# Kernel optimization log

Measured on AMD Instinct MI355X. Metric: run time of the kernel, lower is better.

The kernel has to match this reference:

```python
import jax, jax.numpy as jnp
import numpy as np

N, IN_DIM, HID, OUT_DIM, H = 4096, 256, 256, 256, 2
E_RAND = 131072
BN_EPS = 1e-5


def _bn(h, gamma, beta):
    # BatchNorm1d training-mode math: batch mean, biased variance
    mu = jnp.mean(h, axis=0)
    var = jnp.var(h, axis=0)
    return (h - mu) * jax.lax.rsqrt(var + BN_EPS) * gamma + beta


def setup_inputs() -> dict:
    key = jax.random.key(0)
    ks = jax.random.split(key, 16)
    x = jax.random.normal(ks[0], (N, IN_DIM), jnp.float32)
    # random edges + self loops (self loops guarantee every row has >=1 neighbor)
    rnd = jax.random.randint(ks[1], (2, E_RAND), 0, N, jnp.int64)
    loops = jnp.stack([jnp.arange(N, dtype=jnp.int64)] * 2)
    edge_index = jnp.concatenate([rnd, loops], axis=1)
    s = 1.0 / np.sqrt(IN_DIM)
    sh = 1.0 / np.sqrt(HID)
    return {
        "x": x,
        "edge_index": edge_index,
        "wq": jax.random.uniform(ks[2], (IN_DIM, HID), jnp.float32, -s, s),
        "bq": jnp.zeros((HID,), jnp.float32),
        "wk": jax.random.uniform(ks[3], (IN_DIM, HID), jnp.float32, -s, s),
        "bk": jnp.zeros((HID,), jnp.float32),
        "wv": jax.random.uniform(ks[4], (IN_DIM, HID), jnp.float32, -s, s),
        "bv": jnp.zeros((HID,), jnp.float32),
        "wo": jax.random.uniform(ks[5], (HID, IN_DIM), jnp.float32, -sh, sh),
        "bo": jnp.zeros((IN_DIM,), jnp.float32),
        "eps": jnp.zeros((1, 1), jnp.float32),
        "w1": jax.random.uniform(ks[6], (IN_DIM, HID), jnp.float32, -s, s),
        "b1": jnp.zeros((HID,), jnp.float32),
        "g1": jnp.ones((HID,), jnp.float32),
        "be1": jnp.zeros((HID,), jnp.float32),
        "w2": jax.random.uniform(ks[7], (HID, OUT_DIM), jnp.float32, -sh, sh),
        "b2": jnp.zeros((OUT_DIM,), jnp.float32),
        "g2": jnp.ones((OUT_DIM,), jnp.float32),
        "be2": jnp.zeros((OUT_DIM,), jnp.float32),
    }


def reference(x, edge_index, wq, bq, wk, bk, wv, bv, wo, bo, eps,
              w1, b1, g1, be1, w2, b2, g2, be2):
    n = x.shape[0]
    hd = HID // H
    q = (x @ wq + bq).reshape(n, H, hd)
    k = (x @ wk + bk).reshape(n, H, hd)
    v = (x @ wv + bv).reshape(n, H, hd)
    scores = jnp.einsum('nhd,mhd->nhm', q, k) / (hd ** 0.5)  # [n,H,n]
    row, col = edge_index[0], edge_index[1]
    mask = jnp.zeros((n, H, n), bool).at[row, :, col].set(True)
    scores = jnp.where(mask, scores, -jnp.inf)
    attn = jax.nn.softmax(scores, axis=-1)
    v_agg = jnp.einsum('nhm,mhd->nhd', attn, v).reshape(n, HID)
    v_agg = v_agg @ wo + bo + eps * x
    h = jax.nn.relu(_bn(v_agg @ w1 + b1, g1, be1))
    h = jax.nn.relu(_bn(h @ w2 + b2, g2, be2))
    return h  # dropout is identity (eval)
```

## Files before the change

### kernel.cpp

```cpp
#include <hip/hip_runtime.h>
#include <math.h>

#define N_NODES 4096
#define DIM 256
#define GK 256
#define MWORDS 128
#define MAXNBR 192

typedef float f32x4 __attribute__((ext_vector_type(4)));
typedef short s16x8 __attribute__((ext_vector_type(8)));
typedef short s16x4 __attribute__((ext_vector_type(4)));

__device__ __forceinline__ unsigned short bf16_rne(float f) {
  unsigned int u = __float_as_uint(f);
  u += 0x7FFFu + ((u >> 16) & 1u);
  return (unsigned short)(u >> 16);
}

__device__ __forceinline__ void split_bf16(float f, short& hi, short& lo) {
  unsigned short h = bf16_rne(f);
  float hf = __uint_as_float(((unsigned int)h) << 16);
  hi = (short)h;
  lo = (short)bf16_rne(f - hf);
}

__device__ __forceinline__ int swz(int row, int col) {
  return row * 64 + (col ^ ((row & 7) << 3));
}

__global__ void prep_kernel(const int* __restrict__ ei, int E, int nmb,
                            unsigned int* __restrict__ mask,
                            const float* __restrict__ wq, const float* __restrict__ wk,
                            const float* __restrict__ wv, const float* __restrict__ wo,
                            const float* __restrict__ w1, const float* __restrict__ w2,
                            const float* __restrict__ bq, const float* __restrict__ bk,
                            const float* __restrict__ bv,
                            short* __restrict__ wt_hi, short* __restrict__ wt_lo,
                            float* __restrict__ bqkv, float* __restrict__ stats) {
  const int b = blockIdx.x;
  const int t = threadIdx.x;
  if (b < nmb) {
    const int e = b * 256 + t;
    if (e < E) {
      const int r = ei[e];
      const int c = ei[E + e];
      atomicOr(&mask[(size_t)r * MWORDS + (c >> 5)], 1u << (c & 31));
    }
    return;
  }
  const int b2 = b - nmb;
  if (b2 < 1536) {
    const int mat = b2 >> 8;
    const int n = b2 & 255;
    const float* src = (mat == 0) ? wq : (mat == 1) ? wk : (mat == 2) ? wv
                     : (mat == 3) ? wo : (mat == 4) ? w1 : w2;
    const float v = src[(size_t)t * 256 + n];
    short hi, lo;
    split_bf16(v, hi, lo);
    const int nbase = (mat < 3) ? mat * 256 : 768 + (mat - 3) * 256;
    const size_t idx = (size_t)(nbase + n) * GK + t;
    wt_hi[idx] = hi;
    wt_lo[idx] = lo;
    if (t == 0 && mat < 3)
      bqkv[mat * 256 + n] = (mat == 0 ? bq : mat == 1 ? bk : bv)[n];
    return;
  }
  stats[t] = 0.f;
  stats[t + 256] = 0.f;
  stats[t + 512] = 0.f;
  stats[t + 768] = 0.f;
}

template <int EPI, bool BN_IN, bool STATS_OUT>
__launch_bounds__(256)
__global__ void gemm_mfma(const float* __restrict__ A,
                          const short* __restrict__ Wt_hi,
                          const short* __restrict__ Wt_lo,
                          const float* __restrict__ bias,
                          float* __restrict__ C, int ldc,
                          const float* __restrict__ X,
                          const float* __restrict__ epsp,
                          const float* __restrict__ bnsum,
                          const float* __restrict__ bnsq,
                          const float* __restrict__ bng,
                          const float* __restrict__ bnbe,
                          float* __restrict__ osum,
                          float* __restrict__ osq) {
  __shared__ short As_hi[64 * 64], As_lo[64 * 64];
  __shared__ short Bs_hi[64 * 64], Bs_lo[64 * 64];
  __shared__ __align__(16) float bnsc[256], bnsh[256];
  __shared__ float redS[2][2][16], redQ[2][2][16];

  const int tid = threadIdx.x;
  const int lane = tid & 63;
  const int wave = tid >> 6;
  const int wr = wave >> 1, wc = wave & 1;
  const int m0 = blockIdx.y * 64;
  const int n0 = blockIdx.x * 64;
  const int l15 = lane & 15;
  const int lg = lane >> 4;

  if (BN_IN) {
    const float invn = 1.f / (float)N_NODES;
    const float mu = bnsum[tid] * invn;
    const float var = bnsq[tid] * invn - mu * mu;
    const float s = bng[tid] * rsqrtf(var + 1e-5f);
    bnsc[tid] = s;
    bnsh[tid] = fmaf(-mu, s, bnbe[tid]);
  }

  f32x4 acc[2][2] = {};

  for (int kt = 0; kt < GK; kt += 64) {
    __syncthreads();
#pragma unroll
    for (int i = 0; i < 4; ++i) {
      const int row = (tid >> 4) + i * 16;
      const int kc = (tid & 15) * 4;
      float4 av = *(const float4*)(A + (size_t)(m0 + row) * GK + kt + kc);
      if (EPI == 2) {
        const float4 s4 = *(const float4*)&bnsc[kt + kc];
        const float4 h4 = *(const float4*)&bnsh[kt + kc];
        av.x = fmaxf(fmaf(av.x, s4.x, h4.x), 0.f);
        av.y = fmaxf(fmaf(av.y, s4.y, h4.y), 0.f);
        av.z = fmaxf(fmaf(av.z, s4.z, h4.z), 0.f);
        av.w = fmaxf(fmaf(av.w, s4.w, h4.w), 0.f);
      }
      short h0, l0, h1, l1, h2, l2, h3, l3;
      split_bf16(av.x, h0, l0);
      split_bf16(av.y, h1, l1);
      split_bf16(av.z, h2, l2);
      split_bf16(av.w, h3, l3);
      s16x4 hv = {h0, h1, h2, h3};
      s16x4 lv = {l0, l1, l2, l3};
      const int o = swz(row, kc);
      *(s16x4*)&As_hi[o] = hv;
      *(s16x4*)&As_lo[o] = lv;
    }
#pragma unroll
    for (int i = 0; i < 2; ++i) {
      const int row = (tid >> 3) + i * 32;
      const int kc = (tid & 7) * 8;
      s16x8 bh = *(const s16x8*)(Wt_hi + (size_t)(n0 + row) * GK + kt + kc);
      s16x8 bl = *(const s16x8*)(Wt_lo + (size_t)(n0 + row) * GK + kt + kc);
      const int o = swz(row, kc);
      *(s16x8*)&Bs_hi[o] = bh;
      *(s16x8*)&Bs_lo[o] = bl;
    }
    __syncthreads();
#pragma unroll
    for (int kk = 0; kk < 2; ++kk) {
      s16x8 ah[2], al[2], bh[2], bl[2];
#pragma unroll
      for (int f = 0; f < 2; ++f) {
        const int ao = swz(wr * 32 + f * 16 + l15, kk * 32 + lg * 8);
        const int bo = swz(wc * 32 + f * 16 + l15, kk * 32 + lg * 8);
        ah[f] = *(const s16x8*)&As_hi[ao];
        al[f] = *(const s16x8*)&As_lo[ao];
        bh[f] = *(const s16x8*)&Bs_hi[bo];
        bl[f] = *(const s16x8*)&Bs_lo[bo];
      }
#pragma unroll
      for (int fm = 0; fm < 2; ++fm)
#pragma unroll
        for (int fn = 0; fn < 2; ++fn) {
          acc[fm][fn] = __builtin_amdgcn_mfma_f32_16x16x32_bf16(ah[fm], bh[fn], acc[fm][fn], 0, 0, 0);
          acc[fm][fn] = __builtin_amdgcn_mfma_f32_16x16x32_bf16(ah[fm], bl[fn], acc[fm][fn], 0, 0, 0);
          acc[fm][fn] = __builtin_amdgcn_mfma_f32_16x16x32_bf16(al[fm], bh[fn], acc[fm][fn], 0, 0, 0);
        }
    }
  }

  const float ev = (EPI == 1) ? epsp[0] : 0.f;
  float ps[2] = {0.f, 0.f}, pq[2] = {0.f, 0.f};
#pragma unroll
  for (int fm = 0; fm < 2; ++fm) {
    const int row0 = m0 + wr * 32 + fm * 16 + lg * 4;
#pragma unroll
    for (int fn = 0; fn < 2; ++fn) {
      const int col = n0 + wc * 32 + fn * 16 + l15;
      const float bb = bias[col];
#pragma unroll
      for (int j = 0; j < 4; ++j) {
        float v = acc[fm][fn][j] + bb;
        if (EPI == 1) v = fmaf(ev, X[(size_t)(row0 + j) * DIM + col], v);
        C[(size_t)(row0 + j) * ldc + col] = v;
        if (STATS_OUT) {
          ps[fn] += v;
          pq[fn] = fmaf(v, v, pq[fn]);
        }
      }
    }
  }
  if (STATS_OUT) {
#pragma unroll
    for (int fn = 0; fn < 2; ++fn) {
      ps[fn] += __shfl_xor(ps[fn], 16);
      ps[fn] += __shfl_xor(ps[fn], 32);
      pq[fn] += __shfl_xor(pq[fn], 16);
      pq[fn] += __shfl_xor(pq[fn], 32);
    }
    if (wr == 1 && lane < 16) {
      redS[wc][0][l15] = ps[0];
      redS[wc][1][l15] = ps[1];
      redQ[wc][0][l15] = pq[0];
      redQ[wc][1][l15] = pq[1];
    }
    __syncthreads();
    if (wr == 0 && lane < 16) {
#pragma unroll
      for (int fn = 0; fn < 2; ++fn) {
        const int col = n0 + wc * 32 + fn * 16 + l15;
        atomicAdd(&osum[col], ps[fn] + redS[wc][fn][l15]);
        atomicAdd(&osq[col], pq[fn] + redQ[wc][fn][l15]);
      }
    }
  }
}

__launch_bounds__(256)
__global__ void attn_kernel(const float* __restrict__ qkv,
                            const unsigned int* __restrict__ mask,
                            float* __restrict__ vagg) {
  __shared__ int nbr[4][MAXNBR];
  const int wave = threadIdx.x >> 6;
  const int lane = threadIdx.x & 63;
  const int r = blockIdx.x * 4 + wave;

  const unsigned int* mrow = mask + (size_t)r * MWORDS;
  int total = 0;
#pragma unroll
  for (int round = 0; round < 2; ++round) {
    unsigned int w = mrow[round * 64 + lane];
    const int cnt = __popc(w);
    int pre = cnt;
#pragma unroll
    for (int off = 1; off < 64; off <<= 1) {
      int tt = __shfl_up(pre, off);
      if (lane >= off) pre += tt;
    }
    const int wtot = __shfl(pre, 63);
    pre -= cnt;
    int base = total + pre;
    while (w) {
      const int b = __ffs(w) - 1;
      w &= w - 1;
      nbr[wave][base++] = (round * 64 + lane) * 32 + b;
    }
    total += wtot;
  }

  float4 q = *(const float4*)(qkv + (size_t)r * 768 + lane * 4);
  const float sc = 0.088388347648318447f;
  q.x *= sc; q.y *= sc; q.z *= sc; q.w *= sc;

  float4 acc = make_float4(0.f, 0.f, 0.f, 0.f);
  float m = -INFINITY, lsum = 0.f;
  const int* nb = nbr[wave];

  for (int i = 0; i < total; i += 8) {
    int cs[8];
    float4 kf[8], vf[8];
    float d[8];
#pragma unroll
    for (int j = 0; j < 8; ++j)
      cs[j] = (i + j < total) ? nb[i + j] : -1;
#pragma unroll
    for (int j = 0; j < 8; ++j) {
      const float* p = qkv + (size_t)(cs[j] < 0 ? cs[0] : cs[j]) * 768 + lane * 4;
      kf[j] = *(const float4*)(p + 256);
      vf[j] = *(const float4*)(p + 512);
    }
#pragma unroll
    for (int j = 0; j < 8; ++j)
      d[j] = q.x * kf[j].x + q.y * kf[j].y + q.z * kf[j].z + q.w * kf[j].w;
#pragma unroll
    for (int s = 16; s >= 1; s >>= 1)
#pragma unroll
      for (int j = 0; j < 8; ++j) d[j] += __shfl_xor(d[j], s);
#pragma unroll
    for (int j = 1; j < 8; ++j)
      if (cs[j] < 0) d[j] = -INFINITY;
    float mnew = m;
#pragma unroll
    for (int j = 0; j < 8; ++j) mnew = fmaxf(mnew, d[j]);
    const float resc = __expf(m - mnew);
    float e[8];
    float esum = 0.f;
#pragma unroll
    for (int j = 0; j < 8; ++j) {
      e[j] = __expf(d[j] - mnew);
      esum += e[j];
    }
    lsum = lsum * resc + esum;
    float ax = acc.x * resc, ay = acc.y * resc, az = acc.z * resc, aw = acc.w * resc;
#pragma unroll
    for (int j = 0; j < 8; ++j) {
      ax = fmaf(e[j], vf[j].x, ax);
      ay = fmaf(e[j], vf[j].y, ay);
      az = fmaf(e[j], vf[j].z, az);
      aw = fmaf(e[j], vf[j].w, aw);
    }
    acc.x = ax; acc.y = ay; acc.z = az; acc.w = aw;
    m = mnew;
  }
  const float inv = 1.f / lsum;
  float4 o = make_float4(acc.x * inv, acc.y * inv, acc.z * inv, acc.w * inv);
  *(float4*)(vagg + (size_t)r * DIM + lane * 4) = o;
}

__launch_bounds__(256)
__global__ void bn_apply_final(const float* __restrict__ H,
                               const float* __restrict__ sum,
                               const float* __restrict__ sumsq,
                               const float* __restrict__ g,
                               const float* __restrict__ be,
                               float* __restrict__ out) {
  const int t = threadIdx.x;
  const int c0 = (t * 4) & (DIM - 1);
  const float invn = 1.f / (float)N_NODES;
  float4 s4 = *(const float4*)&sum[c0];
  float4 q4 = *(const float4*)&sumsq[c0];
  float4 g4 = *(const float4*)&g[c0];
  float4 b4 = *(const float4*)&be[c0];
  float scl[4], shf[4];
#pragma unroll
  for (int j = 0; j < 4; ++j) {
    const float mu = ((const float*)&s4)[j] * invn;
    const float var = ((const float*)&q4)[j] * invn - mu * mu;
    const float s = ((const float*)&g4)[j] * rsqrtf(var + 1e-5f);
    scl[j] = s;
    shf[j] = fmaf(-mu, s, ((const float*)&b4)[j]);
  }
  const int stride = gridDim.x * 256;
  for (int i = blockIdx.x * 256 + t; i < N_NODES * DIM / 4; i += stride) {
    const float4 h = ((const float4*)H)[i];
    float4 o;
    o.x = fmaxf(fmaf(h.x, scl[0], shf[0]), 0.f);
    o.y = fmaxf(fmaf(h.y, scl[1], shf[1]), 0.f);
    o.z = fmaxf(fmaf(h.z, scl[2], shf[2]), 0.f);
    o.w = fmaxf(fmaf(h.w, scl[3], shf[3]), 0.f);
    ((float4*)out)[i] = o;
  }
}

extern "C" void kernel_launch(void* const* d_in, const int* in_sizes, int n_in,
                              void* d_out, int out_size, void* d_ws, size_t ws_size,
                              hipStream_t stream) {
  const float* x   = (const float*)d_in[0];
  const int*   ei  = (const int*)d_in[1];
  const float* wq  = (const float*)d_in[2];
  const float* bq  = (const float*)d_in[3];
  const float* wk  = (const float*)d_in[4];
  const float* bk  = (const float*)d_in[5];
  const float* wv  = (const float*)d_in[6];
  const float* bv  = (const float*)d_in[7];
  const float* wo  = (const float*)d_in[8];
  const float* bo  = (const float*)d_in[9];
  const float* eps = (const float*)d_in[10];
  const float* w1  = (const float*)d_in[11];
  const float* b1  = (const float*)d_in[12];
  const float* g1  = (const float*)d_in[13];
  const float* be1 = (const float*)d_in[14];
  const float* w2  = (const float*)d_in[15];
  const float* b2  = (const float*)d_in[16];
  const float* g2  = (const float*)d_in[17];
  const float* be2 = (const float*)d_in[18];
  float* out = (float*)d_out;

  char* ws = (char*)d_ws;
  unsigned int* mask = (unsigned int*)ws;
  size_t off = (size_t)N_NODES * MWORDS * 4;
  short* wt_hi = (short*)(ws + off); off += (size_t)1536 * GK * 2;
  short* wt_lo = (short*)(ws + off); off += (size_t)1536 * GK * 2;
  float* bqkv  = (float*)(ws + off); off += 768 * 4;
  float* stats = (float*)(ws + off); off += 1024 * 4;
  off = (off + 255) & ~(size_t)255;
  float* qkv  = (float*)(ws + off); off += (size_t)N_NODES * 768 * 4;
  float* vagg = (float*)(ws + off); off += (size_t)N_NODES * DIM * 4;
  float* a1   = (float*)(ws + off); off += (size_t)N_NODES * DIM * 4;
  float* h1   = (float*)(ws + off); off += (size_t)N_NODES * DIM * 4;
  float* h2   = (float*)(ws + off); off += (size_t)N_NODES * DIM * 4;

  float* sum1 = stats;
  float* sq1  = stats + 256;
  float* sum2 = stats + 512;
  float* sq2  = stats + 768;

  const int E = in_sizes[1] / 2;
  const int nmb = (E + 255) / 256;

  hipMemsetAsync(mask, 0, (size_t)N_NODES * MWORDS * 4, stream);
  prep_kernel<<<nmb + 1537, 256, 0, stream>>>(ei, E, nmb, mask,
                                              wq, wk, wv, wo, w1, w2,
                                              bq, bk, bv, wt_hi, wt_lo, bqkv, stats);

  dim3 gq(768 / 64, N_NODES / 64);
  gemm_mfma<0, false, false><<<gq, 256, 0, stream>>>(
      x, wt_hi, wt_lo, bqkv, qkv, 768,
      nullptr, nullptr, nullptr, nullptr, nullptr, nullptr, nullptr, nullptr);

  attn_kernel<<<N_NODES / 4, 256, 0, stream>>>(qkv, mask, vagg);

  dim3 gg(DIM / 64, N_NODES / 64);
  gemm_mfma<1, false, false><<<gg, 256, 0, stream>>>(
      vagg, wt_hi + (size_t)768 * GK, wt_lo + (size_t)768 * GK, bo, a1, DIM,
      x, eps, nullptr, nullptr, nullptr, nullptr, nullptr, nullptr);
  gemm_mfma<0, false, true><<<gg, 256, 0, stream>>>(
      a1, wt_hi + (size_t)1024 * GK, wt_lo + (size_t)1024 * GK, b1, h1, DIM,
      nullptr, nullptr, nullptr, nullptr, nullptr, nullptr, sum1, sq1);
  gemm_mfma<2, true, true><<<gg, 256, 0, stream>>>(
      h1, wt_hi + (size_t)1280 * GK, wt_lo + (size_t)1280 * GK, b2, h2, DIM,
      nullptr, nullptr, sum1, sq1, g1, be1, sum2, sq2);
  bn_apply_final<<<512, 256, 0, stream>>>(h2, sum2, sq2, g2, be2, out);
}
```

Before: 166.8 us.

## Fuse mask build into QKV GEMM, pre-split operands to bf16 hi/lo

Mask zeroing moves from hipMemsetAsync into the prep kernel. The edge-to-bitmask atomics move into the QKV GEMM kernel, so they overlap with the GEMM instead of needing their own blocks. The prep kernel now transposes weights through a shared-memory tile so writes coalesce, and it pre-splits x into bf16 hi/lo. The attention and projection kernels write their outputs already split into hi/lo, so downstream GEMMs skip the per-tile conversion and read half-width data. The cost is extra workspace, extra scattered short stores in the epilogues, and atomics inside the GEMM grid that must finish before attention runs.

```diff
diff --git a/kernel.cpp b/kernel.cpp
--- a/kernel.cpp
+++ b/kernel.cpp
@@ -28,121 +28,73 @@
   return row * 64 + (col ^ ((row & 7) << 3));
 }
 
-__global__ void prep_kernel(const int* __restrict__ ei, int E, int nmb,
-                            unsigned int* __restrict__ mask,
-                            const float* __restrict__ wq, const float* __restrict__ wk,
-                            const float* __restrict__ wv, const float* __restrict__ wo,
-                            const float* __restrict__ w1, const float* __restrict__ w2,
-                            const float* __restrict__ bq, const float* __restrict__ bk,
-                            const float* __restrict__ bv,
-                            short* __restrict__ wt_hi, short* __restrict__ wt_lo,
-                            float* __restrict__ bqkv, float* __restrict__ stats) {
-  const int b = blockIdx.x;
-  const int t = threadIdx.x;
-  if (b < nmb) {
-    const int e = b * 256 + t;
-    if (e < E) {
-      const int r = ei[e];
-      const int c = ei[E + e];
-      atomicOr(&mask[(size_t)r * MWORDS + (c >> 5)], 1u << (c & 31));
-    }
-    return;
-  }
-  const int b2 = b - nmb;
-  if (b2 < 1536) {
-    const int mat = b2 >> 8;
-    const int n = b2 & 255;
-    const float* src = (mat == 0) ? wq : (mat == 1) ? wk : (mat == 2) ? wv
-                     : (mat == 3) ? wo : (mat == 4) ? w1 : w2;
-    const float v = src[(size_t)t * 256 + n];
-    short hi, lo;
-    split_bf16(v, hi, lo);
-    const int nbase = (mat < 3) ? mat * 256 : 768 + (mat - 3) * 256;
-    const size_t idx = (size_t)(nbase + n) * GK + t;
-    wt_hi[idx] = hi;
-    wt_lo[idx] = lo;
-    if (t == 0 && mat < 3)
-      bqkv[mat * 256 + n] = (mat == 0 ? bq : mat == 1 ? bk : bv)[n];
-    return;
-  }
-  stats[t] = 0.f;
-  stats[t + 256] = 0.f;
-  stats[t + 512] = 0.f;
-  stats[t + 768] = 0.f;
-}
-
-template <int EPI, bool BN_IN, bool STATS_OUT>
-__launch_bounds__(256)
-__global__ void gemm_mfma(const float* __restrict__ A,
-                          const short* __restrict__ Wt_hi,
-                          const short* __restrict__ Wt_lo,
-                          const float* __restrict__ bias,
-                          float* __restrict__ C, int ldc,
-                          const float* __restrict__ X,
-                          const float* __restrict__ epsp,
-                          const float* __restrict__ bnsum,
-                          const float* __restrict__ bnsq,
-                          const float* __restrict__ bng,
-                          const float* __restrict__ bnbe,
-                          float* __restrict__ osum,
-                          float* __restrict__ osq) {
-  __shared__ short As_hi[64 * 64], As_lo[64 * 64];
-  __shared__ short Bs_hi[64 * 64], Bs_lo[64 * 64];
-  __shared__ __align__(16) float bnsc[256], bnsh[256];
-  __shared__ float redS[2][2][16], redQ[2][2][16];
-
+template <int EPI, bool PRESPLIT, bool WRITE_C, bool SPLIT_OUT, bool STATS_OUT>
+__device__ __forceinline__ void gemm_core(
+    short* As_hi, short* As_lo, short* Bs_hi, short* Bs_lo, float* red,
+    const float* bnsc, const float* bnsh,
+    const float* __restrict__ Af, const short* __restrict__ A_hi,
+    const short* __restrict__ A_lo,
+    const short* __restrict__ Wt_hi, const short* __restrict__ Wt_lo,
+    const float* __restrict__ bias, float* __restrict__ C, int ldc,
+    short* __restrict__ C_hi, short* __restrict__ C_lo,
+    int m0, int n0, const float* __restrict__ X, float ev,
+    float* __restrict__ osum, float* __restrict__ osq) {
   const int tid = threadIdx.x;
   const int lane = tid & 63;
   const int wave = tid >> 6;
   const int wr = wave >> 1, wc = wave & 1;
-  const int m0 = blockIdx.y * 64;
-  const int n0 = blockIdx.x * 64;
   const int l15 = lane & 15;
   const int lg = lane >> 4;
 
-  if (BN_IN) {
-    const float invn = 1.f / (float)N_NODES;
-    const float mu = bnsum[tid] * invn;
-    const float var = bnsq[tid] * invn - mu * mu;
-    const float s = bng[tid] * rsqrtf(var + 1e-5f);
-    bnsc[tid] = s;
-    bnsh[tid] = fmaf(-mu, s, bnbe[tid]);
-  }
-
   f32x4 acc[2][2] = {};
 
   for (int kt = 0; kt < GK; kt += 64) {
     __syncthreads();
-#pragma unroll
-    for (int i = 0; i < 4; ++i) {
-      const int row = (tid >> 4) + i * 16;
-      const int kc = (tid & 15) * 4;
-      float4 av = *(const float4*)(A + (size_t)(m0 + row) * GK + kt + kc);
-      if (EPI == 2) {
-        const float4 s4 = *(const float4*)&bnsc[kt + kc];
-        const float4 h4 = *(const float4*)&bnsh[kt + kc];
-        av.x = fmaxf(fmaf(av.x, s4.x, h4.x), 0.f);
-        av.y = fmaxf(fmaf(av.y, s4.y, h4.y), 0.f);
-        av.z = fmaxf(fmaf(av.z, s4.z, h4.z), 0.f);
-        av.w = fmaxf(fmaf(av.w, s4.w, h4.w), 0.f);
+    if (PRESPLIT) {
+#pragma unroll
+      for (int i = 0; i < 2; ++i) {
+        const int row = (tid >> 3) + i * 32;
+        const int kc = (tid & 7) * 8;
+        const size_t g = (size_t)(m0 + row) * GK + kt + kc;
+        s16x8 ah = *(const s16x8*)(A_hi + g);
+        s16x8 al = *(const s16x8*)(A_lo + g);
+        const int o = swz(row, kc);
+        *(s16x8*)&As_hi[o] = ah;
+        *(s16x8*)&As_lo[o] = al;
       }
-      short h0, l0, h1, l1, h2, l2, h3, l3;
-      split_bf16(av.x, h0, l0);
-      split_bf16(av.y, h1, l1);
-      split_bf16(av.z, h2, l2);
-      split_bf16(av.w, h3, l3);
-      s16x4 hv = {h0, h1, h2, h3};
-      s16x4 lv = {l0, l1, l2, l3};
-      const int o = swz(row, kc);
-      *(s16x4*)&As_hi[o] = hv;
-      *(s16x4*)&As_lo[o] = lv;
+    } else {
+#pragma unroll
+      for (int i = 0; i < 4; ++i) {
+        const int row = (tid >> 4) + i * 16;
+        const int kc = (tid & 15) * 4;
+        float4 av = *(const float4*)(Af + (size_t)(m0 + row) * GK + kt + kc);
+        if (EPI == 2) {
+          const float4 s4 = *(const float4*)&bnsc[kt + kc];
+          const float4 h4 = *(const float4*)&bnsh[kt + kc];
+          av.x = fmaxf(fmaf(av.x, s4.x, h4.x), 0.f);
+          av.y = fmaxf(fmaf(av.y, s4.y, h4.y), 0.f);
+          av.z = fmaxf(fmaf(av.z, s4.z, h4.z), 0.f);
+          av.w = fmaxf(fmaf(av.w, s4.w, h4.w), 0.f);
+        }
+        short h0, l0, h1, l1, h2, l2, h3, l3;
+        split_bf16(av.x, h0, l0);
+        split_bf16(av.y, h1, l1);
+        split_bf16(av.z, h2, l2);
+        split_bf16(av.w, h3, l3);
+        s16x4 hv = {h0, h1, h2, h3};
+        s16x4 lv = {l0, l1, l2, l3};
+        const int o = swz(row, kc);
+        *(s16x4*)&As_hi[o] = hv;
+        *(s16x4*)&As_lo[o] = lv;
+      }
     }
 #pragma unroll
     for (int i = 0; i < 2; ++i) {
       const int row = (tid >> 3) + i * 32;
       const int kc = (tid & 7) * 8;
-      s16x8 bh = *(const s16x8*)(Wt_hi + (size_t)(n0 + row) * GK + kt + kc);
-      s16x8 bl = *(const s16x8*)(Wt_lo + (size_t)(n0 + row) * GK + kt + kc);
+      const size_t g = (size_t)(n0 + row) * GK + kt + kc;
+      s16x8 bh = *(const s16x8*)(Wt_hi + g);
+      s16x8 bl = *(const s16x8*)(Wt_lo + g);
       const int o = swz(row, kc);
       *(s16x8*)&Bs_hi[o] = bh;
       *(s16x8*)&Bs_lo[o] = bl;
@@ -171,7 +123,6 @@
     }
   }
 
-  const float ev = (EPI == 1) ? epsp[0] : 0.f;
   float ps[2] = {0.f, 0.f}, pq[2] = {0.f, 0.f};
 #pragma unroll
   for (int fm = 0; fm < 2; ++fm) {
@@ -184,7 +135,13 @@
       for (int j = 0; j < 4; ++j) {
         float v = acc[fm][fn][j] + bb;
         if (EPI == 1) v = fmaf(ev, X[(size_t)(row0 + j) * DIM + col], v);
-        C[(size_t)(row0 + j) * ldc + col] = v;
+        if (WRITE_C) C[(size_t)(row0 + j) * ldc + col] = v;
+        if (SPLIT_OUT) {
+          short hi, lo;
+          split_bf16(v, hi, lo);
+          C_hi[(size_t)(row0 + j) * DIM + col] = hi;
+          C_lo[(size_t)(row0 + j) * DIM + col] = lo;
+        }
         if (STATS_OUT) {
           ps[fn] += v;
           pq[fn] = fmaf(v, v, pq[fn]);
@@ -193,6 +150,8 @@
     }
   }
   if (STATS_OUT) {
+    float* redS = red;
+    float* redQ = red + 64;
 #pragma unroll
     for (int fn = 0; fn < 2; ++fn) {
       ps[fn] += __shfl_xor(ps[fn], 16);
@@ -201,27 +160,111 @@
       pq[fn] += __shfl_xor(pq[fn], 32);
     }
     if (wr == 1 && lane < 16) {
-      redS[wc][0][l15] = ps[0];
-      redS[wc][1][l15] = ps[1];
-      redQ[wc][0][l15] = pq[0];
-      redQ[wc][1][l15] = pq[1];
+      redS[(wc * 2 + 0) * 16 + l15] = ps[0];
+      redS[(wc * 2 + 1) * 16 + l15] = ps[1];
+      redQ[(wc * 2 + 0) * 16 + l15] = pq[0];
+      redQ[(wc * 2 + 1) * 16 + l15] = pq[1];
     }
     __syncthreads();
     if (wr == 0 && lane < 16) {
 #pragma unroll
       for (int fn = 0; fn < 2; ++fn) {
         const int col = n0 + wc * 32 + fn * 16 + l15;
-        atomicAdd(&osum[col], ps[fn] + redS[wc][fn][l15]);
-        atomicAdd(&osq[col], pq[fn] + redQ[wc][fn][l15]);
+        atomicAdd(&osum[col], ps[fn] + redS[(wc * 2 + fn) * 16 + l15]);
+        atomicAdd(&osq[col], pq[fn] + redQ[(wc * 2 + fn) * 16 + l15]);
       }
     }
   }
 }
 
-__launch_bounds__(256)
-__global__ void attn_kernel(const float* __restrict__ qkv,
-                            const unsigned int* __restrict__ mask,
-                            float* __restrict__ vagg) {
+__global__ __launch_bounds__(256) void k_prep(
+    const float* __restrict__ x,
+    const float* __restrict__ wq, const float* __restrict__ wk,
+    const float* __restrict__ wv, const float* __restrict__ wo,
+    const float* __restrict__ w1, const float* __restrict__ w2,
+    const float* __restrict__ bq, const float* __restrict__ bk,
+    const float* __restrict__ bv,
+    unsigned int* __restrict__ mask, short* __restrict__ wt_hi,
+    short* __restrict__ wt_lo, short* __restrict__ x_hi,
+    short* __restrict__ x_lo, float* __restrict__ bqkv,
+    float* __restrict__ stats) {
+  __shared__ float tr[64][65];
+  const int bid = blockIdx.x;
+  const int tid = threadIdx.x;
+
+  mask[bid * 512 + tid] = 0u;
+  mask[bid * 512 + 256 + tid] = 0u;
+
+  if (bid < 96) {
+    const int mat = bid >> 4;
+    const int tile = bid & 15;
+    const int ti = tile >> 2;
+    const int tj = tile & 3;
+    const float* src = (mat == 0) ? wq : (mat == 1) ? wk : (mat == 2) ? wv
+                     : (mat == 3) ? wo : (mat == 4) ? w1 : w2;
+#pragma unroll
+    for (int q = 0; q < 16; ++q) {
+      const int r = q * 4 + (tid >> 6);
+      tr[r][tid & 63] = src[(size_t)(ti * 64 + r) * 256 + tj * 64 + (tid & 63)];
+    }
+    __syncthreads();
+    const int nbase = (mat < 3) ? mat * 256 : 768 + (mat - 3) * 256;
+#pragma unroll
+    for (int q = 0; q < 16; ++q) {
+      const int n = q * 4 + (tid >> 6);
+      const int k = tid & 63;
+      short hi, lo;
+      split_bf16(tr[k][n], hi, lo);
+      const size_t idx = (size_t)(nbase + tj * 64 + n) * GK + ti * 64 + k;
+      wt_hi[idx] = hi;
+      wt_lo[idx] = lo;
+    }
+  } else if (bid < 608) {
+    const int r0 = (bid - 96) * 8;
+#pragma unroll
+    for (int r = 0; r < 8; ++r) {
+      const size_t g = (size_t)(r0 + r) * 256 + tid;
+      short hi, lo;
+      split_bf16(x[g], hi, lo);
+      x_hi[g] = hi;
+      x_lo[g] = lo;
+    }
+  } else if (bid == 608) {
+    stats[tid] = 0.f;
+    stats[tid + 256] = 0.f;
+    stats[tid + 512] = 0.f;
+    stats[tid + 768] = 0.f;
+  } else if (bid >= 609 && bid < 612) {
+    const int mat = bid - 609;
+    bqkv[mat * 256 + tid] = (mat == 0 ? bq : mat == 1 ? bk : bv)[tid];
+  }
+}
+
+__global__ __launch_bounds__(256) void k_qkv(
+    const short* __restrict__ x_hi, const short* __restrict__ x_lo,
+    const short* __restrict__ wt_hi, const short* __restrict__ wt_lo,
+    const float* __restrict__ bqkv, float* __restrict__ qkv,
+    const int* __restrict__ ei, int E, unsigned int* __restrict__ mask) {
+  __shared__ __align__(16) short As_hi[4096], As_lo[4096], Bs_hi[4096], Bs_lo[4096];
+  {
+    const int blin = blockIdx.y * 12 + blockIdx.x;
+    const int epb = (E + 767) / 768;
+    const int e = blin * epb + threadIdx.x;
+    if (threadIdx.x < epb && e < E) {
+      const int r = ei[e];
+      const int c = ei[E + e];
+      atomicOr(&mask[(size_t)r * MWORDS + (c >> 5)], 1u << (c & 31));
+    }
+  }
+  gemm_core<0, true, true, false, false>(
+      As_hi, As_lo, Bs_hi, Bs_lo, nullptr, nullptr, nullptr,
+      nullptr, x_hi, x_lo, wt_hi, wt_lo, bqkv, qkv, 768, nullptr, nullptr,
+      blockIdx.y * 64, blockIdx.x * 64, nullptr, 0.f, nullptr, nullptr);
+}
+
+__global__ __launch_bounds__(256) void k_attn(
+    const float* __restrict__ qkv, const unsigned int* __restrict__ mask,
+    short* __restrict__ vagg_hi, short* __restrict__ vagg_lo) {
   __shared__ int nbr[4][MAXNBR];
   const int wave = threadIdx.x >> 6;
   const int lane = threadIdx.x & 63;
@@ -253,7 +296,6 @@
   float4 q = *(const float4*)(qkv + (size_t)r * 768 + lane * 4);
   const float sc = 0.088388347648318447f;
   q.x *= sc; q.y *= sc; q.z *= sc; q.w *= sc;
-
   float4 acc = make_float4(0.f, 0.f, 0.f, 0.f);
   float m = -INFINITY, lsum = 0.f;
   const int* nb = nbr[wave];
@@ -263,13 +305,12 @@
     float4 kf[8], vf[8];
     float d[8];
 #pragma unroll
-    for (int j = 0; j < 8; ++j)
-      cs[j] = (i + j < total) ? nb[i + j] : -1;
+    for (int j = 0; j < 8; ++j) cs[j] = (i + j < total) ? nb[i + j] : -1;
 #pragma unroll
     for (int j = 0; j < 8; ++j) {
-      const float* p = qkv + (size_t)(cs[j] < 0 ? cs[0] : cs[j]) * 768 + lane * 4;
-      kf[j] = *(const float4*)(p + 256);
-      vf[j] = *(const float4*)(p + 512);
+      const float* pp = qkv + (size_t)(cs[j] < 0 ? cs[0] : cs[j]) * 768 + lane * 4;
+      kf[j] = *(const float4*)(pp + 256);
+      vf[j] = *(const float4*)(pp + 512);
     }
 #pragma unroll
     for (int j = 0; j < 8; ++j)
@@ -285,8 +326,7 @@
 #pragma unroll
     for (int j = 0; j < 8; ++j) mnew = fmaxf(mnew, d[j]);
     const float resc = __expf(m - mnew);
-    float e[8];
-    float esum = 0.f;
+    float e[8], esum = 0.f;
 #pragma unroll
     for (int j = 0; j < 8; ++j) {
       e[j] = __expf(d[j] - mnew);
@@ -305,17 +345,70 @@
     m = mnew;
   }
   const float inv = 1.f / lsum;
-  float4 o = make_float4(acc.x * inv, acc.y * inv, acc.z * inv, acc.w * inv);
-  *(float4*)(vagg + (size_t)r * DIM + lane * 4) = o;
-}
-
-__launch_bounds__(256)
-__global__ void bn_apply_final(const float* __restrict__ H,
-                               const float* __restrict__ sum,
-                               const float* __restrict__ sumsq,
-                               const float* __restrict__ g,
-                               const float* __restrict__ be,
-                               float* __restrict__ out) {
+  const float o[4] = {acc.x * inv, acc.y * inv, acc.z * inv, acc.w * inv};
+  short hs[4], ls[4];
+#pragma unroll
+  for (int j = 0; j < 4; ++j) split_bf16(o[j], hs[j], ls[j]);
+  const size_t g = (size_t)r * DIM + lane * 4;
+  *(s16x4*)(vagg_hi + g) = *(s16x4*)hs;
+  *(s16x4*)(vagg_lo + g) = *(s16x4*)ls;
+}
+
+__global__ __launch_bounds__(256) void k_proj(
+    const short* __restrict__ vagg_hi, const short* __restrict__ vagg_lo,
+    const short* __restrict__ wt_hi, const short* __restrict__ wt_lo,
+    const float* __restrict__ bo, const float* __restrict__ x,
+    const float* __restrict__ epsp,
+    short* __restrict__ a1_hi, short* __restrict__ a1_lo) {
+  __shared__ __align__(16) short As_hi[4096], As_lo[4096], Bs_hi[4096], Bs_lo[4096];
+  gemm_core<1, true, false, true, false>(
+      As_hi, As_lo, Bs_hi, Bs_lo, nullptr, nullptr, nullptr,
+      nullptr, vagg_hi, vagg_lo, wt_hi, wt_lo, bo, nullptr, DIM, a1_hi, a1_lo,
+      blockIdx.y * 64, blockIdx.x * 64, x, epsp[0], nullptr, nullptr);
+}
+
+__global__ __launch_bounds__(256) void k_mlp1(
+    const short* __restrict__ a1_hi, const short* __restrict__ a1_lo,
+    const short* __restrict__ wt_hi, const short* __restrict__ wt_lo,
+    const float* __restrict__ b1, float* __restrict__ h1,
+    float* __restrict__ osum, float* __restrict__ osq) {
+  __shared__ __align__(16) short As_hi[4096], As_lo[4096], Bs_hi[4096], Bs_lo[4096];
+  __shared__ float red[128];
+  gemm_core<0, true, true, false, true>(
+      As_hi, As_lo, Bs_hi, Bs_lo, red, nullptr, nullptr,
+      nullptr, a1_hi, a1_lo, wt_hi, wt_lo, b1, h1, DIM, nullptr, nullptr,
+      blockIdx.y * 64, blockIdx.x * 64, nullptr, 0.f, osum, osq);
+}
+
+__global__ __launch_bounds__(256) void k_mlp2(
+    const float* __restrict__ h1,
+    const short* __restrict__ wt_hi, const short* __restrict__ wt_lo,
+    const float* __restrict__ b2,
+    const float* __restrict__ bnsum, const float* __restrict__ bnsq,
+    const float* __restrict__ g1, const float* __restrict__ be1,
+    float* __restrict__ h2, float* __restrict__ osum, float* __restrict__ osq) {
+  __shared__ __align__(16) short As_hi[4096], As_lo[4096], Bs_hi[4096], Bs_lo[4096];
+  __shared__ __align__(16) float bnsc[256], bnsh[256];
+  __shared__ float red[128];
+  const int tid = threadIdx.x;
+  {
+    const float invn = 1.f / (float)N_NODES;
+    const float mu = bnsum[tid] * invn;
+    const float var = bnsq[tid] * invn - mu * mu;
+    const float s = g1[tid] * rsqrtf(var + 1e-5f);
+    bnsc[tid] = s;
+    bnsh[tid] = fmaf(-mu, s, be1[tid]);
+  }
+  gemm_core<2, false, true, false, true>(
+      As_hi, As_lo, Bs_hi, Bs_lo, red, bnsc, bnsh,
+      h1, nullptr, nullptr, wt_hi, wt_lo, b2, h2, DIM, nullptr, nullptr,
+      blockIdx.y * 64, blockIdx.x * 64, nullptr, 0.f, osum, osq);
+}
+
+__global__ __launch_bounds__(256) void k_bnfinal(
+    const float* __restrict__ H, const float* __restrict__ sum,
+    const float* __restrict__ sumsq, const float* __restrict__ g,
+    const float* __restrict__ be, float* __restrict__ out) {
   const int t = threadIdx.x;
   const int c0 = (t * 4) & (DIM - 1);
   const float invn = 1.f / (float)N_NODES;
@@ -373,44 +466,38 @@
   size_t off = (size_t)N_NODES * MWORDS * 4;
   short* wt_hi = (short*)(ws + off); off += (size_t)1536 * GK * 2;
   short* wt_lo = (short*)(ws + off); off += (size_t)1536 * GK * 2;
+  short* x_hi  = (short*)(ws + off); off += (size_t)N_NODES * DIM * 2;
+  short* x_lo  = (short*)(ws + off); off += (size_t)N_NODES * DIM * 2;
+  short* vg_hi = (short*)(ws + off); off += (size_t)N_NODES * DIM * 2;
+  short* vg_lo = (short*)(ws + off); off += (size_t)N_NODES * DIM * 2;
+  short* a1_hi = (short*)(ws + off); off += (size_t)N_NODES * DIM * 2;
+  short* a1_lo = (short*)(ws + off); off += (size_t)N_NODES * DIM * 2;
   float* bqkv  = (float*)(ws + off); off += 768 * 4;
   float* stats = (float*)(ws + off); off += 1024 * 4;
   off = (off + 255) & ~(size_t)255;
-  float* qkv  = (float*)(ws + off); off += (size_t)N_NODES * 768 * 4;
-  float* vagg = (float*)(ws + off); off += (size_t)N_NODES * DIM * 4;
-  float* a1   = (float*)(ws + off); off += (size_t)N_NODES * DIM * 4;
-  float* h1   = (float*)(ws + off); off += (size_t)N_NODES * DIM * 4;
-  float* h2   = (float*)(ws + off); off += (size_t)N_NODES * DIM * 4;
-
-  float* sum1 = stats;
-  float* sq1  = stats + 256;
-  float* sum2 = stats + 512;
-  float* sq2  = stats + 768;
+  float* qkv = (float*)(ws + off); off += (size_t)N_NODES * 768 * 4;
+  float* h1  = (float*)(ws + off); off += (size_t)N_NODES * DIM * 4;
+  float* h2  = (float*)(ws + off); off += (size_t)N_NODES * DIM * 4;
 
   const int E = in_sizes[1] / 2;
-  const int nmb = (E + 255) / 256;
-
-  hipMemsetAsync(mask, 0, (size_t)N_NODES * MWORDS * 4, stream);
-  prep_kernel<<<nmb + 1537, 256, 0, stream>>>(ei, E, nmb, mask,
-                                              wq, wk, wv, wo, w1, w2,
-                                              bq, bk, bv, wt_hi, wt_lo, bqkv, stats);
-
-  dim3 gq(768 / 64, N_NODES / 64);
-  gemm_mfma<0, false, false><<<gq, 256, 0, stream>>>(
-      x, wt_hi, wt_lo, bqkv, qkv, 768,
-      nullptr, nullptr, nullptr, nullptr, nullptr, nullptr, nullptr, nullptr);
-
-  attn_kernel<<<N_NODES / 4, 256, 0, stream>>>(qkv, mask, vagg);
-
-  dim3 gg(DIM / 64, N_NODES / 64);
-  gemm_mfma<1, false, false><<<gg, 256, 0, stream>>>(
-      vagg, wt_hi + (size_t)768 * GK, wt_lo + (size_t)768 * GK, bo, a1, DIM,
-      x, eps, nullptr, nullptr, nullptr, nullptr, nullptr, nullptr);
-  gemm_mfma<0, false, true><<<gg, 256, 0, stream>>>(
-      a1, wt_hi + (size_t)1024 * GK, wt_lo + (size_t)1024 * GK, b1, h1, DIM,
-      nullptr, nullptr, nullptr, nullptr, nullptr, nullptr, sum1, sq1);
-  gemm_mfma<2, true, true><<<gg, 256, 0, stream>>>(
-      h1, wt_hi + (size_t)1280 * GK, wt_lo + (size_t)1280 * GK, b2, h2, DIM,
-      nullptr, nullptr, sum1, sq1, g1, be1, sum2, sq2);
-  bn_apply_final<<<512, 256, 0, stream>>>(h2, sum2, sq2, g2, be2, out);
-}
+
+  k_prep<<<1024, 256, 0, stream>>>(x, wq, wk, wv, wo, w1, w2, bq, bk, bv,
+                                   mask, wt_hi, wt_lo, x_hi, x_lo, bqkv, stats);
+  k_qkv<<<dim3(12, 64), 256, 0, stream>>>(x_hi, x_lo, wt_hi, wt_lo, bqkv, qkv,
+                                          ei, E, mask);
+  k_attn<<<N_NODES / 4, 256, 0, stream>>>(qkv, mask, vg_hi, vg_lo);
+  k_proj<<<dim3(4, 64), 256, 0, stream>>>(vg_hi, vg_lo,
+                                          wt_hi + (size_t)768 * GK,
+                                          wt_lo + (size_t)768 * GK,
+                                          bo, x, eps, a1_hi, a1_lo);
+  k_mlp1<<<dim3(4, 64), 256, 0, stream>>>(a1_hi, a1_lo,
+                                          wt_hi + (size_t)1024 * GK,
+                                          wt_lo + (size_t)1024 * GK,
+                                          b1, h1, stats, stats + 256);
+  k_mlp2<<<dim3(4, 64), 256, 0, stream>>>(h1,
+                                          wt_hi + (size_t)1280 * GK,
+                                          wt_lo + (size_t)1280 * GK,
+                                          b2, stats, stats + 256, g1, be1,
+                                          h2, stats + 512, stats + 768);
+  k_bnfinal<<<512, 256, 0, stream>>>(h2, stats + 512, stats + 768, g2, be2, out);
+}
```

Result: faster. 162.3 us (-2.7%).
